# Performance work log

Measured on AMD Instinct MI355X. Metric: run time of the kernel, lower is better.

The kernel has to match this reference:

```python
import jax, jax.numpy as jnp
import numpy as np

K = 20          # num neighbors (init kwarg k)
BN_EPS = 1e-5   # PyTorch BatchNorm default eps


def setup_inputs() -> dict:
    key = jax.random.key(0)
    k1, k2 = jax.random.split(key, 2)
    x = jax.random.normal(k1, (8, 64, 4096), dtype=jnp.float32)       # (b, d, n)
    w = jax.random.normal(k2, (64, 128), dtype=jnp.float32) * 0.05    # Conv2d 1x1: (out=64, in=2*64)
    gamma = jnp.ones((64,), jnp.float32)    # BatchNorm1d weight
    beta = jnp.zeros((64,), jnp.float32)    # BatchNorm1d bias
    return {"x": x, "w": w, "gamma": gamma, "beta": beta}


def reference(x, w, gamma, beta):
    # x: (b, d, n)
    xt = jnp.swapaxes(x, 1, 2)                       # (b, n, d)
    # kNN via pairwise squared euclidean distance (same ordering as torch.cdist)
    sq = jnp.sum(xt * xt, axis=-1)                   # (b, n)
    d2 = sq[:, :, None] + sq[:, None, :] - 2.0 * jnp.einsum('bnd,bmd->bnm', xt, xt)
    _, idx = jax.lax.top_k(-d2, K)                   # (b, n, K) smallest distances
    # gather neighbor features: (b, n, K, d)
    nb = jax.vmap(lambda pts, i: pts[i])(xt, idx)
    ctr = xt[:, :, None, :]                          # (b, n, 1, d)
    # edge feature = concat([neighbor - x, x]) -> (b, n, K, 2d)
    feat = jnp.concatenate([nb - ctr, jnp.broadcast_to(ctr, nb.shape)], axis=-1)
    # 1x1 conv (no bias) then max over neighbors
    h = jnp.max(jnp.einsum('bnkc,oc->bnko', feat, w), axis=2)   # (b, n, out)
    # BatchNorm1d (training mode: batch statistics over (b, n), biased var)
    mean = jnp.mean(h, axis=(0, 1))
    var = jnp.mean((h - mean) ** 2, axis=(0, 1))
    hn = (h - mean) / jnp.sqrt(var + BN_EPS) * gamma + beta
    out = jax.nn.gelu(hn, approximate=False)         # exact GELU (PyTorch default)
    return jnp.swapaxes(out, 1, 2)                   # (b, out, n)
```

## Files before the change

### kernel.cpp

```cpp
#include <hip/hip_runtime.h>

#define BIGF 3.402823466e38f

typedef __attribute__((ext_vector_type(8))) short bf16x8;
typedef __attribute__((ext_vector_type(4))) float f32x4;

__device__ __forceinline__ void gload_lds16u(const unsigned short* g, unsigned short* lds) {
  __builtin_amdgcn_global_load_lds((const __attribute__((address_space(1))) void*)g,
                                   (__attribute__((address_space(3))) void*)lds, 16, 0, 0);
}

__device__ __forceinline__ unsigned short bf16_rne(float f) {
  unsigned int u = __float_as_uint(f);
  return (unsigned short)((u + 0x7fffu + ((u >> 16) & 1u)) >> 16);
}

__global__ __launch_bounds__(256) void k1_pre(const float* __restrict__ x, const float* __restrict__ w,
                                              float* __restrict__ sq, float* __restrict__ y,
                                              float* __restrict__ delta, unsigned short* __restrict__ xhl) {
  __shared__ __align__(16) float xt[64][68];
  __shared__ __align__(16) float ws[128][64];
  const int t = threadIdx.x;
  const int bid = blockIdx.x;
  const int b = bid >> 6;
  const int n0 = (bid & 63) << 6;
  const float* xb = x + (size_t)b * 64 * 4096;

#pragma unroll
  for (int rep = 0; rep < 16; ++rep) {
    int id = rep * 256 + t;
    int d = id >> 6, n = id & 63;
    xt[n][d] = xb[(size_t)d * 4096 + n0 + n];
  }
#pragma unroll
  for (int rep = 0; rep < 32; ++rep) {
    int id = rep * 256 + t;
    int u = id >> 6, dd = id & 63;
    ws[u][dd] = w[(u & 63) * 128 + ((u >> 6) << 6) + dd];
  }
  __syncthreads();

  {
    const int p = t >> 2;
    const int cg = t & 3;
    uint4* orow = (uint4*)xhl + ((size_t)(b << 12) + n0 + p) * 16;
#pragma unroll
    for (int cc = 0; cc < 4; ++cc) {
      const int c = cg * 4 + cc;
      const int kb = (c & 7) * 8;
      const bool lohalf = (c >= 8);
      unsigned int pk[4];
#pragma unroll
      for (int j2 = 0; j2 < 4; ++j2) {
        unsigned short u0, u1;
#pragma unroll
        for (int e = 0; e < 2; ++e) {
          const float xv = xt[p][kb + j2 * 2 + e];
          unsigned short h = bf16_rne(xv);
          unsigned short r;
          if (!lohalf) r = h;
          else r = bf16_rne(xv - __uint_as_float(((unsigned int)h) << 16));
          if (e == 0) u0 = r; else u1 = r;
        }
        pk[j2] = (unsigned int)u0 | ((unsigned int)u1 << 16);
      }
      uint4 v;
      v.x = pk[0]; v.y = pk[1]; v.z = pk[2]; v.w = pk[3];
      orow[c ^ (p & 7)] = v;
    }
  }

  const int p = t & 63;
  const int oc = t >> 6;
  float accy[16], accz[16];
#pragma unroll
  for (int j = 0; j < 16; ++j) { accy[j] = 0.f; accz[j] = 0.f; }

#pragma unroll 4
  for (int d4 = 0; d4 < 16; ++d4) {
    const float4 xv = *(const float4*)&xt[p][d4 * 4];
#pragma unroll
    for (int j = 0; j < 16; ++j) {
      const int o = oc * 16 + j;
      const float4 wy = *(const float4*)&ws[o][d4 * 4];
      const float4 wz = *(const float4*)&ws[o + 64][d4 * 4];
      accy[j] = fmaf(xv.x, wy.x, fmaf(xv.y, wy.y, fmaf(xv.z, wy.z, fmaf(xv.w, wy.w, accy[j]))));
      accz[j] = fmaf(xv.x, wz.x, fmaf(xv.y, wz.y, fmaf(xv.z, wz.z, fmaf(xv.w, wz.w, accz[j]))));
    }
  }

  if (oc == 0) {
    float s = 0.f;
#pragma unroll
    for (int d4 = 0; d4 < 16; ++d4) {
      const float4 v = *(const float4*)&xt[p][d4 * 4];
      s = fmaf(v.x, v.x, fmaf(v.y, v.y, fmaf(v.z, v.z, fmaf(v.w, v.w, s))));
    }
    sq[b * 4096 + n0 + p] = s;
  }

  const size_t row = ((size_t)b * 4096 + n0 + p) * 64 + oc * 16;
#pragma unroll
  for (int j4 = 0; j4 < 4; ++j4) {
    float4 yv = make_float4(accy[j4 * 4], accy[j4 * 4 + 1], accy[j4 * 4 + 2], accy[j4 * 4 + 3]);
    float4 dv = make_float4(accz[j4 * 4] - accy[j4 * 4], accz[j4 * 4 + 1] - accy[j4 * 4 + 1],
                            accz[j4 * 4 + 2] - accy[j4 * 4 + 2], accz[j4 * 4 + 3] - accy[j4 * 4 + 3]);
    *(float4*)&y[row + j4 * 4] = yv;
    *(float4*)&delta[row + j4 * 4] = dv;
  }
}

__global__ __launch_bounds__(256, 2) void k2_knn(const unsigned short* __restrict__ xhl,
                                                 const float* __restrict__ sq,
                                                 int* __restrict__ idx_out) {
  __shared__ __align__(16) float smem[12352];
  const int t = threadIdx.x;
  const int lane = t & 63;
  const int w = t >> 6;
  float* BsW = smem + 4096 + (w << 11);
  uint4* BsW4 = (uint4*)BsW;
  const uint4* As4 = (const uint4*)smem;
  unsigned* bufD = (unsigned*)smem;
  unsigned* bufI = (unsigned*)(smem + 2048);
  unsigned* thrNa = (unsigned*)(smem + 12288);
  volatile unsigned* thrNv = (volatile unsigned*)(smem + 12288);

  const int bid = blockIdx.x;
  const int b = bid >> 6;
  const int n0 = (bid & 63) << 6;
  const int pn = lane & 15, q = lane >> 4;
  const int myn = lane;
  const int swz = myn & 7;

  const unsigned short* xr = xhl + ((size_t)(b << 12)) * 128;
  const float* sqb = sq + (b << 12);

  if (t < 64) thrNa[t] = 0x7F7FFFFFu;

  {
    unsigned short* asu = (unsigned short*)smem;
#pragma unroll
    for (int qq = 0; qq < 4; ++qq) {
      const int kk = w * 4 + qq;
      gload_lds16u(xr + (size_t)n0 * 128 + kk * 512 + lane * 8, asu + kk * 512);
    }
  }
  const float sqn = sqb[n0 + myn];
  __builtin_amdgcn_s_waitcnt(0x0F70);
  __syncthreads();

  bf16x8 bfr[4][4];
#pragma unroll
  for (int nt = 0; nt < 4; ++nt)
#pragma unroll
    for (int j = 0; j < 4; ++j)
      bfr[nt][j] = *reinterpret_cast<const bf16x8*>(&As4[((nt << 4) + pn) * 16 + (((j << 2) + q) ^ (pn & 7))]);
  __syncthreads();

  float kd[20];
  int ki[20];
#pragma unroll
  for (int s = 0; s < 20; ++s) { kd[s] = BIGF; ki[s] = -1; }
  int cnt = 0;

  auto ins = [&](float vd, int vi) {
#pragma unroll
    for (int s = 0; s < 20; ++s) {
      const float od = kd[s];
      const int oi = ki[s];
      const bool lt = vd < od;
      kd[s] = lt ? vd : od;
      ki[s] = lt ? vi : oi;
      vd = lt ? od : vd;
      vi = lt ? oi : vi;
    }
  };

  auto drain = [&]() {
#pragma unroll 1
    for (int j = 0; j < 8; ++j) {
      if (!__any(j < cnt)) break;
      if (j < cnt) {
        const float dv = __uint_as_float(bufD[j * 256 + t]);
        const int iv = (int)bufI[j * 256 + t];
        if (dv < kd[19]) ins(dv, iv);
      }
    }
    cnt = 0;
    atomicMin(&thrNa[myn], __float_as_uint(kd[19]));
  };

  const f32x4 zero4 = {0.f, 0.f, 0.f, 0.f};
  f32x4 acc[4][2];
#pragma unroll
  for (int nt = 0; nt < 4; ++nt) { acc[nt][0] = zero4; acc[nt][1] = zero4; }

  for (int kt = 0; kt < 32; ++kt) {
    const int mbase = (w + 4 * kt) << 5;
    {
      unsigned short* bsu = (unsigned short*)BsW;
      const unsigned short* src = xr + (size_t)mbase * 128;
#pragma unroll
      for (int k = 0; k < 8; ++k) gload_lds16u(src + k * 512 + lane * 8, bsu + k * 512);
    }
    const f32x4 sqm0 = *(const f32x4*)&sqb[mbase + (q << 2)];
    const f32x4 sqm1 = *(const f32x4*)&sqb[mbase + 16 + (q << 2)];
    __builtin_amdgcn_s_waitcnt(0x0F70);

    float thr2 = (fminf(__uint_as_float(thrNv[myn]), kd[19]) - sqn) + 0.001f;

#pragma unroll
    for (int mt = 0; mt < 2; ++mt) {
      bf16x8 afr[4];
#pragma unroll
      for (int j = 0; j < 4; ++j)
        afr[j] = *reinterpret_cast<const bf16x8*>(&BsW4[((mt << 4) + pn) * 16 + (((j << 2) + q) ^ (pn & 7))]);
#pragma unroll
      for (int nt = 0; nt < 4; ++nt) {
        f32x4 a = acc[nt][mt];
        a = __builtin_amdgcn_mfma_f32_16x16x32_bf16(afr[0], bfr[nt][0], a, 0, 0, 0);
        a = __builtin_amdgcn_mfma_f32_16x16x32_bf16(afr[1], bfr[nt][1], a, 0, 0, 0);
        a = __builtin_amdgcn_mfma_f32_16x16x32_bf16(afr[0], bfr[nt][2], a, 0, 0, 0);
        a = __builtin_amdgcn_mfma_f32_16x16x32_bf16(afr[1], bfr[nt][3], a, 0, 0, 0);
        a = __builtin_amdgcn_mfma_f32_16x16x32_bf16(afr[2], bfr[nt][0], a, 0, 0, 0);
        a = __builtin_amdgcn_mfma_f32_16x16x32_bf16(afr[3], bfr[nt][1], a, 0, 0, 0);
        acc[nt][mt] = a;
      }
    }

#pragma unroll
    for (int nt = 0; nt < 4; ++nt) {
#pragma unroll
      for (int mt = 0; mt < 2; ++mt) {
        const int n = (nt << 4) + pn;
        const int g = (mt << 2) + q;
        const int pc = g ^ (n & 7);
        const f32x4 sv = mt ? sqm1 : sqm0;
        f32x4 dv = sv - 2.0f * acc[nt][mt];
        *(f32x4*)&BsW[(n << 5) + (pc << 2)] = dv;
        acc[nt][mt] = zero4;
      }
    }

#pragma unroll 1
    for (int half = 0; half < 2; ++half) {
      const int cb = half << 2;
      const float4 v0 = *(const float4*)&BsW[(myn << 5) + (((cb + 0) ^ swz) << 2)];
      const float4 v1 = *(const float4*)&BsW[(myn << 5) + (((cb + 1) ^ swz) << 2)];
      const float4 v2 = *(const float4*)&BsW[(myn << 5) + (((cb + 2) ^ swz) << 2)];
      const float4 v3 = *(const float4*)&BsW[(myn << 5) + (((cb + 3) ^ swz) << 2)];
#pragma unroll
      for (int cc = 0; cc < 4; ++cc) {
        const float4 v = (cc == 0) ? v0 : (cc == 1) ? v1 : (cc == 2) ? v2 : v3;
        const int mb = mbase + ((cb + cc) << 2);
        const float mn = fminf(fminf(v.x, v.y), fminf(v.z, v.w));
        if (mn < thr2) {
          if (v.x < thr2) { bufD[cnt * 256 + t] = __float_as_uint(sqn + v.x); bufI[cnt * 256 + t] = (unsigned)mb; cnt++; }
          if (v.y < thr2) { bufD[cnt * 256 + t] = __float_as_uint(sqn + v.y); bufI[cnt * 256 + t] = (unsigned)(mb + 1); cnt++; }
          if (v.z < thr2) { bufD[cnt * 256 + t] = __float_as_uint(sqn + v.z); bufI[cnt * 256 + t] = (unsigned)(mb + 2); cnt++; }
          if (v.w < thr2) { bufD[cnt * 256 + t] = __float_as_uint(sqn + v.w); bufI[cnt * 256 + t] = (unsigned)(mb + 3); cnt++; }
        }
        if (__any(cnt > 4)) {
          drain();
          thr2 = fminf(thr2, (fminf(__uint_as_float(thrNv[myn]), kd[19]) - sqn) + 0.001f);
        }
      }
    }
  }
  drain();

  __syncthreads();
  float* pf = smem;
  int* pi = (int*)(smem + 5120);
#pragma unroll
  for (int s = 0; s < 20; ++s) {
    pf[(w * 20 + s) * 64 + lane] = kd[s];
    pi[(w * 20 + s) * 64 + lane] = ki[s];
  }
  __syncthreads();
  if (w == 0) {
    auto insTie = [&](float vd, int vi) {
#pragma unroll
      for (int s = 0; s < 20; ++s) {
        const float od = kd[s];
        const int oi = ki[s];
        const bool lt = (vd < od) || (vd == od && vi < oi);
        kd[s] = lt ? vd : od;
        ki[s] = lt ? vi : oi;
        vd = lt ? od : vd;
        vi = lt ? oi : vi;
      }
    };
    for (int ww = 1; ww < 4; ++ww) {
#pragma unroll 1
      for (int s = 0; s < 20; ++s) {
        const float dv = pf[(ww * 20 + s) * 64 + lane];
        const int iv = pi[(ww * 20 + s) * 64 + lane];
        if (dv < kd[19] || (dv == kd[19] && iv < ki[19])) insTie(dv, iv);
      }
    }
    int* orow = idx_out + ((size_t)(b << 12) + n0 + lane) * 20;
#pragma unroll
    for (int s = 0; s < 20; ++s) orow[s] = ki[s];
  }
}

__global__ __launch_bounds__(256) void k3_gather(const float* __restrict__ y,
                                                 const float* __restrict__ delta,
                                                 const int* __restrict__ idx,
                                                 float* __restrict__ h,
                                                 float* __restrict__ sums,
                                                 float* __restrict__ sumsq) {
  const int t = threadIdx.x;
  const int lane = t & 63;
  const int w = t >> 6;
  const int blk = blockIdx.x;
  float s1 = 0.f, s2 = 0.f;
  for (int p = 0; p < 16; ++p) {
    const int ng = blk * 64 + w * 16 + p;
    const int b = ng >> 12;
    const int* row = idx + (size_t)ng * 20;
    float mx = -BIGF;
#pragma unroll
    for (int kk = 0; kk < 20; ++kk) {
      const int nbr = row[kk];
      mx = fmaxf(mx, y[((size_t)(b << 12) + nbr) * 64 + lane]);
    }
    const float hv = mx + delta[(size_t)ng * 64 + lane];
    h[(size_t)ng * 64 + lane] = hv;
    s1 += hv;
    s2 += hv * hv;
  }
  __shared__ float r1[4][64], r2[4][64];
  r1[w][lane] = s1;
  r2[w][lane] = s2;
  __syncthreads();
  if (w == 0) {
    const float a = r1[0][lane] + r1[1][lane] + r1[2][lane] + r1[3][lane];
    const float c = r2[0][lane] + r2[1][lane] + r2[2][lane] + r2[3][lane];
    atomicAdd(&sums[lane], a);
    atomicAdd(&sumsq[lane], c);
  }
}

__global__ __launch_bounds__(256) void k4_bn(const float* __restrict__ h,
                                             const float* __restrict__ sums,
                                             const float* __restrict__ sumsq,
                                             const float* __restrict__ gamma,
                                             const float* __restrict__ beta,
                                             float* __restrict__ out) {
  __shared__ float tile[64][65];
  const int bid = blockIdx.x;
  const int b = bid >> 6;
  const int n0 = (bid & 63) << 6;
  const int t = threadIdx.x;
  const int o = t & 63;
#pragma unroll
  for (int it = 0; it < 16; ++it) {
    const int n = (t >> 6) * 16 + it;
    tile[n][o] = h[(((size_t)b << 12) + n0 + n) * 64 + o];
  }
  __syncthreads();
  const int j = t & 63;
#pragma unroll
  for (int it = 0; it < 16; ++it) {
    const int oo = (t >> 6) * 16 + it;
    const float mean = sums[oo] * (1.0f / 32768.0f);
    const float var = sumsq[oo] * (1.0f / 32768.0f) - mean * mean;
    const float sc = gamma[oo] / sqrtf(var + 1e-5f);
    const float hv = tile[j][oo];
    const float hn = (hv - mean) * sc + beta[oo];
    const float g = 0.5f * hn * (1.0f + erff(hn * 0.70710678118654752f));
    out[((size_t)(b * 64 + oo)) * 4096 + n0 + j] = g;
  }
}

extern "C" void kernel_launch(void* const* d_in, const int* in_sizes, int n_in,
                              void* d_out, int out_size, void* d_ws, size_t ws_size,
                              hipStream_t stream) {
  const float* x = (const float*)d_in[0];
  const float* w = (const float*)d_in[1];
  const float* gamma = (const float*)d_in[2];
  const float* beta = (const float*)d_in[3];
  float* out = (float*)d_out;

  float* sq_ws = (float*)d_ws;
  float* y_ws = sq_ws + 32768;
  float* delta_ws = y_ws + 2097152;
  float* h_ws = delta_ws + 2097152;
  int* idx_ws = (int*)(h_ws + 2097152);
  float* sums = (float*)(idx_ws + 655360);
  float* sumsq = sums + 64;
  unsigned short* xhl = (unsigned short*)h_ws;

  hipMemsetAsync(sums, 0, 2 * 64 * sizeof(float), stream);
  k1_pre<<<512, 256, 0, stream>>>(x, w, sq_ws, y_ws, delta_ws, xhl);
  k2_knn<<<512, 256, 0, stream>>>(xhl, sq_ws, idx_ws);
  k3_gather<<<512, 256, 0, stream>>>(y_ws, delta_ws, idx_ws, h_ws, sums, sumsq);
  k4_bn<<<512, 256, 0, stream>>>(h_ws, sums, sumsq, gamma, beta, out);
}
```

Baseline: 352.8 us.

## Process 64-candidate tiles per wave in kNN with separate candidate buffer

Each wave in the kNN kernel now handles a 64-candidate tile per iteration instead of 32, which halves the outer loop count and the global-to-LDS load rounds per candidate. The distance tile uses a wider XOR swizzle to match. The candidate buffer moves into its own LDS region so it no longer aliases the staging area. It is shortened to 6 slots and drained when any lane holds more than 2 entries. LDS use rises considerably, which with launch_bounds(256,2) may limit occupancy, and the earlier drain threshold may cause more frequent drains.

```diff
diff --git a/kernel.cpp b/kernel.cpp
--- a/kernel.cpp
+++ b/kernel.cpp
@@ -113,24 +113,24 @@
 __global__ __launch_bounds__(256, 2) void k2_knn(const unsigned short* __restrict__ xhl,
                                                  const float* __restrict__ sq,
                                                  int* __restrict__ idx_out) {
-  __shared__ __align__(16) float smem[12352];
+  __shared__ __align__(16) float smem[19520];
   const int t = threadIdx.x;
   const int lane = t & 63;
   const int w = t >> 6;
-  float* BsW = smem + 4096 + (w << 11);
-  uint4* BsW4 = (uint4*)BsW;
+  float* stW = smem + (w << 12);
+  const uint4* St4 = (const uint4*)stW;
   const uint4* As4 = (const uint4*)smem;
-  unsigned* bufD = (unsigned*)smem;
-  unsigned* bufI = (unsigned*)(smem + 2048);
-  unsigned* thrNa = (unsigned*)(smem + 12288);
-  volatile unsigned* thrNv = (volatile unsigned*)(smem + 12288);
+  unsigned* bufD = (unsigned*)(smem + 16384);
+  unsigned* bufI = (unsigned*)(smem + 17920);
+  unsigned* thrNa = (unsigned*)(smem + 19456);
+  volatile unsigned* thrNv = (volatile unsigned*)(smem + 19456);
 
   const int bid = blockIdx.x;
   const int b = bid >> 6;
   const int n0 = (bid & 63) << 6;
   const int pn = lane & 15, q = lane >> 4;
   const int myn = lane;
-  const int swz = myn & 7;
+  const int swz = myn & 15;
 
   const unsigned short* xr = xhl + ((size_t)(b << 12)) * 128;
   const float* sqb = sq + (b << 12);
@@ -178,7 +178,7 @@
 
   auto drain = [&]() {
 #pragma unroll 1
-    for (int j = 0; j < 8; ++j) {
+    for (int j = 0; j < 6; ++j) {
       if (!__any(j < cnt)) break;
       if (j < cnt) {
         const float dv = __uint_as_float(bufD[j * 256 + t]);
@@ -191,33 +191,32 @@
   };
 
   const f32x4 zero4 = {0.f, 0.f, 0.f, 0.f};
-  f32x4 acc[4][2];
-#pragma unroll
-  for (int nt = 0; nt < 4; ++nt) { acc[nt][0] = zero4; acc[nt][1] = zero4; }
-
-  for (int kt = 0; kt < 32; ++kt) {
-    const int mbase = (w + 4 * kt) << 5;
+
+  for (int kt = 0; kt < 16; ++kt) {
+    const int mbase = (w + (kt << 2)) << 6;
     {
-      unsigned short* bsu = (unsigned short*)BsW;
+      unsigned short* stu = (unsigned short*)stW;
       const unsigned short* src = xr + (size_t)mbase * 128;
 #pragma unroll
-      for (int k = 0; k < 8; ++k) gload_lds16u(src + k * 512 + lane * 8, bsu + k * 512);
-    }
-    const f32x4 sqm0 = *(const f32x4*)&sqb[mbase + (q << 2)];
-    const f32x4 sqm1 = *(const f32x4*)&sqb[mbase + 16 + (q << 2)];
+      for (int k = 0; k < 16; ++k) gload_lds16u(src + k * 512 + lane * 8, stu + k * 512);
+    }
+    f32x4 sqm[4];
+#pragma unroll
+    for (int mt = 0; mt < 4; ++mt) sqm[mt] = *(const f32x4*)&sqb[mbase + (mt << 4) + (q << 2)];
     __builtin_amdgcn_s_waitcnt(0x0F70);
 
     float thr2 = (fminf(__uint_as_float(thrNv[myn]), kd[19]) - sqn) + 0.001f;
 
-#pragma unroll
-    for (int mt = 0; mt < 2; ++mt) {
+    f32x4 acc[4][4];
+#pragma unroll
+    for (int mt = 0; mt < 4; ++mt) {
       bf16x8 afr[4];
 #pragma unroll
       for (int j = 0; j < 4; ++j)
-        afr[j] = *reinterpret_cast<const bf16x8*>(&BsW4[((mt << 4) + pn) * 16 + (((j << 2) + q) ^ (pn & 7))]);
+        afr[j] = *reinterpret_cast<const bf16x8*>(&St4[((mt << 4) + pn) * 16 + (((j << 2) + q) ^ (pn & 7))]);
 #pragma unroll
       for (int nt = 0; nt < 4; ++nt) {
-        f32x4 a = acc[nt][mt];
+        f32x4 a = zero4;
         a = __builtin_amdgcn_mfma_f32_16x16x32_bf16(afr[0], bfr[nt][0], a, 0, 0, 0);
         a = __builtin_amdgcn_mfma_f32_16x16x32_bf16(afr[1], bfr[nt][1], a, 0, 0, 0);
         a = __builtin_amdgcn_mfma_f32_16x16x32_bf16(afr[0], bfr[nt][2], a, 0, 0, 0);
@@ -231,24 +230,22 @@
 #pragma unroll
     for (int nt = 0; nt < 4; ++nt) {
 #pragma unroll
-      for (int mt = 0; mt < 2; ++mt) {
+      for (int mt = 0; mt < 4; ++mt) {
         const int n = (nt << 4) + pn;
         const int g = (mt << 2) + q;
-        const int pc = g ^ (n & 7);
-        const f32x4 sv = mt ? sqm1 : sqm0;
-        f32x4 dv = sv - 2.0f * acc[nt][mt];
-        *(f32x4*)&BsW[(n << 5) + (pc << 2)] = dv;
-        acc[nt][mt] = zero4;
+        const int pc = g ^ (n & 15);
+        f32x4 dv = sqm[mt] - 2.0f * acc[nt][mt];
+        *(f32x4*)&stW[(n << 6) + (pc << 2)] = dv;
       }
     }
 
 #pragma unroll 1
-    for (int half = 0; half < 2; ++half) {
-      const int cb = half << 2;
-      const float4 v0 = *(const float4*)&BsW[(myn << 5) + (((cb + 0) ^ swz) << 2)];
-      const float4 v1 = *(const float4*)&BsW[(myn << 5) + (((cb + 1) ^ swz) << 2)];
-      const float4 v2 = *(const float4*)&BsW[(myn << 5) + (((cb + 2) ^ swz) << 2)];
-      const float4 v3 = *(const float4*)&BsW[(myn << 5) + (((cb + 3) ^ swz) << 2)];
+    for (int g4 = 0; g4 < 4; ++g4) {
+      const int cb = g4 << 2;
+      const float4 v0 = *(const float4*)&stW[(myn << 6) + (((cb + 0) ^ swz) << 2)];
+      const float4 v1 = *(const float4*)&stW[(myn << 6) + (((cb + 1) ^ swz) << 2)];
+      const float4 v2 = *(const float4*)&stW[(myn << 6) + (((cb + 2) ^ swz) << 2)];
+      const float4 v3 = *(const float4*)&stW[(myn << 6) + (((cb + 3) ^ swz) << 2)];
 #pragma unroll
       for (int cc = 0; cc < 4; ++cc) {
         const float4 v = (cc == 0) ? v0 : (cc == 1) ? v1 : (cc == 2) ? v2 : v3;
@@ -260,7 +257,7 @@
           if (v.z < thr2) { bufD[cnt * 256 + t] = __float_as_uint(sqn + v.z); bufI[cnt * 256 + t] = (unsigned)(mb + 2); cnt++; }
           if (v.w < thr2) { bufD[cnt * 256 + t] = __float_as_uint(sqn + v.w); bufI[cnt * 256 + t] = (unsigned)(mb + 3); cnt++; }
         }
-        if (__any(cnt > 4)) {
+        if (__any(cnt > 2)) {
           drain();
           thr2 = fminf(thr2, (fminf(__uint_as_float(thrNv[myn]), kd[19]) - sqn) + 0.001f);
         }
```

Result: slower. 379.4 us (+7.5%).
